# Performance work log

Measured on AMD Instinct MI355X. Metric: run time of the kernel, lower is better.

## Reference

```python
import jax, jax.numpy as jnp
import numpy as np

B, C, H, W = 16, 256, 96, 96
S, N = 128, 64  # num_s = 2*num_mid, num_n = num_mid
EPS = 1e-5


def _bn(x, g, b, m, v):
    # inference-mode BatchNorm2d over channel dim of x:[B,C,H,W]
    scale = g / jnp.sqrt(v + EPS)
    return (x - m[:, None, None]) * scale[:, None, None] + b[:, None, None]


def _proj(x, w, b, g, bb, m, v):
    # 1x1 conv + BN + ReLU (Basconv with is_batchnorm=True, kernel=1)
    y = jnp.einsum('bchw,oc->bohw', x, w) + b[:, None, None]
    return jax.nn.relu(_bn(y, g, bb, m, v))


def _gcn(x, w1, b1, w2):
    # x: [B, S, N]. conv1 acts on node dim (Conv1d over num_node channels),
    # residual add, LeakyReLU(0.2), conv2 acts on state dim (bias=False).
    h = jnp.einsum('bsn,mn->bsm', x, w1) + b1  # node mixing
    h = jax.nn.leaky_relu(h + x, 0.2)
    return jnp.einsum('bsn,ts->btn', h, w2)  # state mixing


def setup_inputs() -> dict:
    key = jax.random.key(0)
    ks = list(jax.random.split(key, 32))
    it = iter(ks)

    def nx(shape, s=0.05):
        return jax.random.normal(next(it), shape, jnp.float32) * s

    inp = {"x": jax.random.normal(next(it), (B, C, H, W), jnp.float32)}
    for name, o in [("s", S), ("p", N), ("r", N)]:
        inp[f"w_{name}"] = nx((o, C))
        inp[f"b_{name}"] = nx((o,))
        inp[f"bn_{name}_g"] = 1.0 + nx((o,))
        inp[f"bn_{name}_b"] = nx((o,))
        inp[f"bn_{name}_m"] = nx((o,))
        inp[f"bn_{name}_v"] = 0.5 + jax.random.uniform(next(it), (o,), jnp.float32)
    inp["g1_w1"] = nx((N, N)); inp["g1_b1"] = nx((N,)); inp["g1_w2"] = nx((S, S))
    inp["g2_w1"] = nx((N, N)); inp["g2_b1"] = nx((N,)); inp["g2_w2"] = nx((S, S))
    inp["fc2_w"] = nx((C, S))
    inp["bn_o_g"] = 1.0 + nx((C,))
    inp["bn_o_b"] = nx((C,))
    inp["bn_o_m"] = nx((C,))
    inp["bn_o_v"] = 0.5 + jax.random.uniform(next(it), (C,), jnp.float32)
    return inp


def reference(x, w_s, b_s, bn_s_g, bn_s_b, bn_s_m, bn_s_v,
              w_p, b_p, bn_p_g, bn_p_b, bn_p_m, bn_p_v,
              w_r, b_r, bn_r_g, bn_r_b, bn_r_m, bn_r_v,
              g1_w1, g1_b1, g1_w2, g2_w1, g2_b1, g2_w2,
              fc2_w, bn_o_g, bn_o_b, bn_o_m, bn_o_v):
    HW = H * W
    xs = _proj(x, w_s, b_s, bn_s_g, bn_s_b, bn_s_m, bn_s_v).reshape(B, S, HW)
    xp = _proj(x, w_p, b_p, bn_p_g, bn_p_b, bn_p_m, bn_p_v).reshape(B, N, HW)
    xr = _proj(x, w_r, b_r, bn_r_g, bn_r_b, bn_r_m, bn_r_v).reshape(B, N, HW)
    # project spatial features into latent graph: [B,S,N], normalized by HW
    g = jnp.einsum('bsl,bnl->bsn', xs, xp) * (1.0 / HW)
    g = _gcn(g, g1_w1, g1_b1, g1_w2)
    g = _gcn(g, g2_w1, g2_b1, g2_w2)
    # reproject latent graph back to spatial: [B,S,HW] -> [B,S,H,W]
    y = jnp.einsum('bsn,bnl->bsl', g, xr).reshape(B, S, H, W)
    y = jnp.einsum('bshw,cs->bchw', y, fc2_w)  # fc_2: 1x1 conv, no bias
    return x + _bn(y, bn_o_g, bn_o_b, bn_o_m, bn_o_v)
```

## Files before the change

### kernel.cpp

```cpp
#include <hip/hip_runtime.h>
#include <cstdint>
#include <cstddef>

#define B_ 16
#define C_ 256
#define HW_ 9216
#define S_ 128
#define N_ 64
#define LT_ 144
#define KSPLIT 12
#define LCHUNK 768

typedef __attribute__((ext_vector_type(8))) short bf16x8;
typedef __attribute__((ext_vector_type(4))) float f32x4;
typedef __attribute__((ext_vector_type(8))) unsigned short u16x8;

__device__ __forceinline__ unsigned short f2bf(float f) {
    unsigned int u = __builtin_bit_cast(unsigned int, f);
    u += 0x7fffu + ((u >> 16) & 1u);
    return (unsigned short)(u >> 16);
}
__device__ __forceinline__ float bf2f(unsigned short u) {
    unsigned int x = ((unsigned int)u) << 16;
    return __builtin_bit_cast(float, x);
}

__global__ void k0_prep(
    const float* __restrict__ w_s, const float* __restrict__ w_p, const float* __restrict__ w_r,
    const float* __restrict__ b_s, const float* __restrict__ g_s, const float* __restrict__ bb_s,
    const float* __restrict__ m_s, const float* __restrict__ v_s,
    const float* __restrict__ b_p, const float* __restrict__ g_p, const float* __restrict__ bb_p,
    const float* __restrict__ m_p, const float* __restrict__ v_p,
    const float* __restrict__ b_r, const float* __restrict__ g_r, const float* __restrict__ bb_r,
    const float* __restrict__ m_r, const float* __restrict__ v_r,
    const float* __restrict__ og, const float* __restrict__ ob,
    const float* __restrict__ om, const float* __restrict__ ov,
    unsigned short* __restrict__ Wcf, float* __restrict__ pscale, float* __restrict__ pbeta,
    float* __restrict__ oscale, float* __restrict__ obeta)
{
    const int gid = blockIdx.x * 256 + threadIdx.x;
    const int oc = gid >> 8, c = gid & 255;
    const float* wsrc;
    if (oc < 128)      wsrc = w_s + oc * 256;
    else if (oc < 192) wsrc = w_p + (oc - 128) * 256;
    else               wsrc = w_r + (oc - 192) * 256;
    Wcf[(c >> 3) * 2048 + oc * 8 + (c & 7)] = f2bf(wsrc[c]);
    if (gid < 256) {
        int i; const float *bp, *gp, *bbp, *mp, *vp;
        if (gid < 128)      { i = gid;       bp = b_s; gp = g_s; bbp = bb_s; mp = m_s; vp = v_s; }
        else if (gid < 192) { i = gid - 128; bp = b_p; gp = g_p; bbp = bb_p; mp = m_p; vp = v_p; }
        else                { i = gid - 192; bp = b_r; gp = g_r; bbp = bb_r; mp = m_r; vp = v_r; }
        const float sc = gp[i] / sqrtf(vp[i] + 1e-5f);
        pscale[gid] = sc;
        pbeta[gid]  = (bp[i] - mp[i]) * sc + bbp[i];
        const float so = og[gid] / sqrtf(ov[gid] + 1e-5f);
        oscale[gid] = so;
        obeta[gid]  = ob[gid] - om[gid] * so;
    }
}

__global__ void k0b_wbf(
    const float* __restrict__ g1w1, const float* __restrict__ g1w2,
    const float* __restrict__ g2w1, const float* __restrict__ g2w2,
    const float* __restrict__ fc2w, unsigned short* __restrict__ wbf)
{
    const int gid = blockIdx.x * 256 + threadIdx.x;
    float v;
    if (gid < 4096)       v = g1w1[gid];
    else if (gid < 20480) v = g1w2[gid - 4096];
    else if (gid < 24576) v = g2w1[gid - 20480];
    else if (gid < 40960) v = g2w2[gid - 24576];
    else                  v = fc2w[gid - 40960];
    wbf[gid] = f2bf(v);
}

__global__ __launch_bounds__(256, 3) void k1_proj(
    const float* __restrict__ x, const unsigned short* __restrict__ Wcf,
    const float* __restrict__ pscale, const float* __restrict__ pbeta,
    unsigned short* __restrict__ xsp, unsigned short* __restrict__ xrt)
{
    __shared__ unsigned short SH[18432];
    const int t = threadIdx.x;
    const int lane = t & 63;
    const int w = t >> 6;
    const int lt = blockIdx.x;
    const int b  = blockIdx.y;
    const int l0 = lt * 64;
    const float* xb = x + (size_t)b * C_ * HW_;
    const int lf = lane & 15;
    const int q4 = lane >> 4;
    const int kg0 = q4 * 8;
    const int r4 = q4 * 4;

    const int lq = t & 15;
    const int cs = t >> 4;
    const int c0 = cs * 4;

    f32x4 acc[4][4] = {};
    f32x4 Breg[4];

    #pragma unroll
    for (int j = 0; j < 4; ++j)
        Breg[j] = *(const f32x4*)(xb + (size_t)(c0 + j) * HW_ + l0 + lq * 4);

    for (int kt = 0; kt < 4; ++kt) {
        unsigned short* buf = SH + (kt & 1) * 4608;
        #pragma unroll
        for (int r = 0; r < 4; ++r) {
            const int ll = lq * 4 + r;
            ushort4 wv;
            wv.x = f2bf(Breg[0][r]); wv.y = f2bf(Breg[1][r]);
            wv.z = f2bf(Breg[2][r]); wv.w = f2bf(Breg[3][r]);
            *(ushort4*)&buf[ll * 72 + (c0 ^ ((lq & 7) << 3))] = wv;
        }
        __syncthreads();
        if (kt < 3) {
            const int k0n = (kt + 1) * 64;
            #pragma unroll
            for (int j = 0; j < 4; ++j)
                Breg[j] = *(const f32x4*)(xb + (size_t)(k0n + c0 + j) * HW_ + l0 + lq * 4);
        }
        #pragma unroll
        for (int ks = 0; ks < 2; ++ks) {
            const int kg = ks * 32 + kg0;
            bf16x8 al[4], bo[4];
            #pragma unroll
            for (int mi = 0; mi < 4; ++mi) {
                const int rr = mi * 16 + lf;
                al[mi] = *(const bf16x8*)&buf[rr * 72 + (kg ^ (((rr >> 2) & 7) << 3))];
            }
            const int chunk = kt * 8 + ks * 4 + q4;
            #pragma unroll
            for (int ni = 0; ni < 4; ++ni)
                bo[ni] = *(const bf16x8*)(Wcf + (size_t)chunk * 2048 + (w * 64 + ni * 16 + lf) * 8);
            #pragma unroll
            for (int mi = 0; mi < 4; ++mi)
                #pragma unroll
                for (int ni = 0; ni < 4; ++ni)
                    acc[mi][ni] = __builtin_amdgcn_mfma_f32_16x16x32_bf16(al[mi], bo[ni], acc[mi][ni], 0, 0, 0);
        }
        __syncthreads();
    }

    if (w < 3) {
        #pragma unroll
        for (int ni = 0; ni < 4; ++ni) {
            const int oc = w * 64 + ni * 16 + lf;
            const float sc = pscale[oc];
            const float bt = pbeta[oc];
            #pragma unroll
            for (int mi = 0; mi < 4; ++mi) {
                const int lcol = mi * 16 + r4;
                ushort4 pk;
                #pragma unroll
                for (int r = 0; r < 4; ++r) {
                    float y = acc[mi][ni][r] * sc + bt;
                    y = y > 0.f ? y : 0.f;
                    ((unsigned short*)&pk)[r] = f2bf(y);
                }
                *(ushort4*)&SH[oc * 72 + lcol] = pk;
            }
        }
    } else {
        #pragma unroll
        for (int ni = 0; ni < 4; ++ni) {
            const int oc = 192 + ni * 16 + lf;
            const float sc = pscale[oc];
            const float bt = pbeta[oc];
            const int n = ni * 16 + lf;
            #pragma unroll
            for (int mi = 0; mi < 4; ++mi) {
                const int lbase = mi * 16 + r4;
                #pragma unroll
                for (int r = 0; r < 4; ++r) {
                    float y = acc[mi][ni][r] * sc + bt;
                    y = y > 0.f ? y : 0.f;
                    xrt[((size_t)b * HW_ + l0 + lbase + r) * 64 + n] = f2bf(y);
                }
            }
        }
    }
    __syncthreads();

    #pragma unroll
    for (int i = 0; i < 6; ++i) {
        const int id = t + i * 256;
        const int row = id >> 3;
        const int c8 = (id & 7) * 8;
        const u16x8 v = *(const u16x8*)&SH[row * 72 + c8];
        *(u16x8*)(xsp + ((size_t)b * 192 + row) * HW_ + l0 + c8) = v;
    }
}

__global__ __launch_bounds__(256) void k2_gram(
    const unsigned short* __restrict__ xsp, float* __restrict__ gpart)
{
    __shared__ unsigned short As[128 * 136];
    __shared__ unsigned short Bs[64 * 136];
    const int t = threadIdx.x;
    const int lane = t & 63;
    const int w = t >> 6;
    const int ck = blockIdx.x;
    const int b = blockIdx.y;

    f32x4 acc[2][4] = {};

    for (int it = 0; it < 6; ++it) {
        const int lg = ck * LCHUNK + it * 128;
        {
            const int rr = t >> 4;
            const int lq2 = (t & 15) * 8;
            #pragma unroll
            for (int i = 0; i < 8; ++i) {
                const int s = rr + 16 * i;
                *(u16x8*)&As[s * 136 + lq2] =
                    *(const u16x8*)(xsp + ((size_t)b * 192 + s) * HW_ + lg + lq2);
            }
            #pragma unroll
            for (int i = 0; i < 4; ++i) {
                const int n = rr + 16 * i;
                *(u16x8*)&Bs[n * 136 + lq2] =
                    *(const u16x8*)(xsp + ((size_t)b * 192 + 128 + n) * HW_ + lg + lq2);
            }
        }
        __syncthreads();
        #pragma unroll
        for (int ks = 0; ks < 4; ++ks) {
            const int kg = ks * 32 + (lane >> 4) * 8;
            bf16x8 a[2], bv[4];
            #pragma unroll
            for (int mi = 0; mi < 2; ++mi)
                a[mi] = *(const bf16x8*)&As[(w * 32 + mi * 16 + (lane & 15)) * 136 + kg];
            #pragma unroll
            for (int ni = 0; ni < 4; ++ni)
                bv[ni] = *(const bf16x8*)&Bs[(ni * 16 + (lane & 15)) * 136 + kg];
            #pragma unroll
            for (int mi = 0; mi < 2; ++mi)
                #pragma unroll
                for (int ni = 0; ni < 4; ++ni)
                    acc[mi][ni] = __builtin_amdgcn_mfma_f32_16x16x32_bf16(a[mi], bv[ni], acc[mi][ni], 0, 0, 0);
        }
        __syncthreads();
    }
    float* gp = gpart + (size_t)(ck * 16 + b) * (S_ * N_);
    const int lf = lane & 15, r4 = (lane >> 4) * 4;
    #pragma unroll
    for (int mi = 0; mi < 2; ++mi)
        #pragma unroll
        for (int ni = 0; ni < 4; ++ni)
            #pragma unroll
            for (int r = 0; r < 4; ++r) {
                const int s = w * 32 + mi * 16 + r4 + r;
                const int n = ni * 16 + lf;
                gp[s * 64 + n] = acc[mi][ni][r];
            }
}

__global__ __launch_bounds__(128) void kred(
    const float* __restrict__ gpart, unsigned short* __restrict__ gred)
{
    const int id = blockIdx.x * 128 + threadIdx.x;
    f32x4 s = {};
    const float* p = gpart + (size_t)id * 4;
    #pragma unroll
    for (int ck = 0; ck < KSPLIT; ++ck)
        s += *(const f32x4*)(p + (size_t)ck * 16 * (S_ * N_));
    s *= (1.0f / (float)HW_);
    ushort4 h;
    h.x = f2bf(s[0]); h.y = f2bf(s[1]); h.z = f2bf(s[2]); h.w = f2bf(s[3]);
    *(ushort4*)&gred[(size_t)id * 4] = h;
}

__global__ __launch_bounds__(256) void k_gcn(
    const unsigned short* __restrict__ gred, const unsigned short* __restrict__ wbf,
    const float* __restrict__ b1a, const float* __restrict__ b1b,
    unsigned short* __restrict__ hc)
{
    __shared__ unsigned short G[128 * 72];
    __shared__ unsigned short HT[64 * 136];
    __shared__ unsigned short T2[64 * 136];
    const int b = blockIdx.x;
    const int t = threadIdx.x;
    const int lane = t & 63;
    const int w = t >> 6;
    const int lf = lane & 15;
    const int kg0 = (lane >> 4) * 8;
    const int r4 = (lane >> 4) * 4;

    const unsigned short* w1a = wbf;
    const unsigned short* w2a = wbf + 4096;
    const unsigned short* w1b = wbf + 20480;
    const unsigned short* w2b = wbf + 24576;
    const unsigned short* fc2 = wbf + 40960;

    #pragma unroll
    for (int i = 0; i < 4; ++i) {
        const int chunk = t + i * 256;
        const u16x8 v = *(const u16x8*)(gred + (size_t)b * (S_ * N_) + chunk * 8);
        const int s = chunk >> 3, n = (chunk & 7) * 8;
        *(u16x8*)&G[s * 72 + n] = v;
    }
    __syncthreads();

    for (int pass = 0; pass < 2; ++pass) {
        const unsigned short* w1 = pass ? w1b : w1a;
        const unsigned short* w2 = pass ? w2b : w2a;
        const float* b1 = pass ? b1b : b1a;

        {
            f32x4 acc[2][4] = {};
            #pragma unroll
            for (int ks = 0; ks < 2; ++ks) {
                const int kg = ks * 32 + kg0;
                bf16x8 a[2], bv[4];
                #pragma unroll
                for (int mi = 0; mi < 2; ++mi)
                    a[mi] = *(const bf16x8*)&G[(w * 32 + mi * 16 + lf) * 72 + kg];
                #pragma unroll
                for (int ni = 0; ni < 4; ++ni)
                    bv[ni] = *(const bf16x8*)(w1 + (ni * 16 + lf) * 64 + kg);
                #pragma unroll
                for (int mi = 0; mi < 2; ++mi)
                    #pragma unroll
                    for (int ni = 0; ni < 4; ++ni)
                        acc[mi][ni] = __builtin_amdgcn_mfma_f32_16x16x32_bf16(a[mi], bv[ni], acc[mi][ni], 0, 0, 0);
            }
            #pragma unroll
            for (int mi = 0; mi < 2; ++mi) {
                const int s0 = w * 32 + mi * 16 + r4;
                #pragma unroll
                for (int ni = 0; ni < 4; ++ni) {
                    const int m = ni * 16 + lf;
                    const float bm = b1[m];
                    ushort4 pk;
                    #pragma unroll
                    for (int r = 0; r < 4; ++r) {
                        float v = acc[mi][ni][r] + bm + bf2f(G[(s0 + r) * 72 + m]);
                        v = v > 0.f ? v : 0.2f * v;
                        ((unsigned short*)&pk)[r] = f2bf(v);
                    }
                    *(ushort4*)&HT[m * 136 + s0] = pk;
                }
            }
        }
        __syncthreads();

        {
            f32x4 acc[2][4] = {};
            #pragma unroll
            for (int ks = 0; ks < 4; ++ks) {
                const int kg = ks * 32 + kg0;
                bf16x8 a[2], bv[4];
                #pragma unroll
                for (int mi = 0; mi < 2; ++mi)
                    a[mi] = *(const bf16x8*)(w2 + (w * 32 + mi * 16 + lf) * 128 + kg);
                #pragma unroll
                for (int ni = 0; ni < 4; ++ni)
                    bv[ni] = *(const bf16x8*)&HT[(ni * 16 + lf) * 136 + kg];
                #pragma unroll
                for (int mi = 0; mi < 2; ++mi)
                    #pragma unroll
                    for (int ni = 0; ni < 4; ++ni)
                        acc[mi][ni] = __builtin_amdgcn_mfma_f32_16x16x32_bf16(a[mi], bv[ni], acc[mi][ni], 0, 0, 0);
            }
            if (pass == 0) {
                #pragma unroll
                for (int mi = 0; mi < 2; ++mi) {
                    const int t0 = w * 32 + mi * 16 + r4;
                    #pragma unroll
                    for (int ni = 0; ni < 4; ++ni) {
                        const int m = ni * 16 + lf;
                        #pragma unroll
                        for (int r = 0; r < 4; ++r)
                            G[(t0 + r) * 72 + m] = f2bf(acc[mi][ni][r]);
                    }
                }
            } else {
                #pragma unroll
                for (int mi = 0; mi < 2; ++mi) {
                    const int t0 = w * 32 + mi * 16 + r4;
                    #pragma unroll
                    for (int ni = 0; ni < 4; ++ni) {
                        const int m = ni * 16 + lf;
                        ushort4 pk;
                        #pragma unroll
                        for (int r = 0; r < 4; ++r)
                            ((unsigned short*)&pk)[r] = f2bf(acc[mi][ni][r]);
                        *(ushort4*)&T2[m * 136 + t0] = pk;
                    }
                }
            }
        }
        __syncthreads();
    }

    {
        f32x4 acc[4][4] = {};
        #pragma unroll
        for (int ks = 0; ks < 4; ++ks) {
            const int kg = ks * 32 + kg0;
            bf16x8 a[4], bv[4];
            #pragma unroll
            for (int mi = 0; mi < 4; ++mi)
                a[mi] = *(const bf16x8*)(fc2 + (w * 64 + mi * 16 + lf) * 128 + kg);
            #pragma unroll
            for (int ni = 0; ni < 4; ++ni)
                bv[ni] = *(const bf16x8*)&T2[(ni * 16 + lf) * 136 + kg];
            #pragma unroll
            for (int mi = 0; mi < 4; ++mi)
                #pragma unroll
                for (int ni = 0; ni < 4; ++ni)
                    acc[mi][ni] = __builtin_amdgcn_mfma_f32_16x16x32_bf16(a[mi], bv[ni], acc[mi][ni], 0, 0, 0);
        }
        #pragma unroll
        for (int mi = 0; mi < 4; ++mi) {
            const int c0 = w * 64 + mi * 16 + r4;
            #pragma unroll
            for (int ni = 0; ni < 4; ++ni) {
                const int n = ni * 16 + lf;
                #pragma unroll
                for (int r = 0; r < 4; ++r)
                    hc[((size_t)b * 256 + c0 + r) * 64 + n] = f2bf(acc[mi][ni][r]);
            }
        }
    }
}

__global__ __launch_bounds__(256) void k3_out(
    const float* __restrict__ x, const unsigned short* __restrict__ hc,
    const unsigned short* __restrict__ xrt,
    const float* __restrict__ oscale, const float* __restrict__ obeta,
    float* __restrict__ out)
{
    const int t = threadIdx.x;
    const int lane = t & 63;
    const int w = t >> 6;
    const int wr = w >> 1, wc = w & 1;
    const int l0 = blockIdx.x * 128;
    const int moff = blockIdx.y * 128;
    const int b = blockIdx.z;
    const int lf = lane & 15;
    const int q4 = lane >> 4;
    const int kg0 = q4 * 8;
    const int r4 = q4 * 4;

    const unsigned short* hb = hc + (size_t)b * 256 * 64 + (size_t)(moff + wr * 64) * 64;
    const unsigned short* xrb = xrt + ((size_t)b * HW_ + l0 + wc * 64) * 64;

    f32x4 acc[4][4] = {};
    #pragma unroll
    for (int ks = 0; ks < 2; ++ks) {
        const int kg = ks * 32 + kg0;
        bf16x8 al[4], bc[4];
        #pragma unroll
        for (int mi = 0; mi < 4; ++mi)
            al[mi] = *(const bf16x8*)(xrb + (size_t)(mi * 16 + lf) * 64 + kg);
        #pragma unroll
        for (int ni = 0; ni < 4; ++ni)
            bc[ni] = *(const bf16x8*)(hb + (size_t)(ni * 16 + lf) * 64 + kg);
        #pragma unroll
        for (int mi = 0; mi < 4; ++mi)
            #pragma unroll
            for (int ni = 0; ni < 4; ++ni)
                acc[mi][ni] = __builtin_amdgcn_mfma_f32_16x16x32_bf16(al[mi], bc[ni], acc[mi][ni], 0, 0, 0);
    }
    #pragma unroll
    for (int ni = 0; ni < 4; ++ni) {
        const int c = moff + wr * 64 + ni * 16 + lf;
        const float sc = oscale[c];
        const float bt = obeta[c];
        const size_t rowb = ((size_t)b * 256 + c) * HW_;
        #pragma unroll
        for (int mi = 0; mi < 4; ++mi) {
            const int l = l0 + wc * 64 + mi * 16 + r4;
            const f32x4 xv = *(const f32x4*)(x + rowb + l);
            f32x4 o;
            #pragma unroll
            for (int r = 0; r < 4; ++r)
                o[r] = xv[r] + acc[mi][ni][r] * sc + bt;
            *(f32x4*)(out + rowb + l) = o;
        }
    }
}

extern "C" void kernel_launch(void* const* d_in, const int* in_sizes, int n_in,
                              void* d_out, int out_size, void* d_ws, size_t ws_size,
                              hipStream_t stream) {
    (void)in_sizes; (void)n_in; (void)out_size;
    const float* x     = (const float*)d_in[0];
    const float* w_s   = (const float*)d_in[1];
    const float* b_s   = (const float*)d_in[2];
    const float* g_s   = (const float*)d_in[3];
    const float* bb_s  = (const float*)d_in[4];
    const float* m_s   = (const float*)d_in[5];
    const float* v_s   = (const float*)d_in[6];
    const float* w_p   = (const float*)d_in[7];
    const float* b_p   = (const float*)d_in[8];
    const float* g_p   = (const float*)d_in[9];
    const float* bb_p  = (const float*)d_in[10];
    const float* m_p   = (const float*)d_in[11];
    const float* v_p   = (const float*)d_in[12];
    const float* w_r   = (const float*)d_in[13];
    const float* b_r   = (const float*)d_in[14];
    const float* g_r   = (const float*)d_in[15];
    const float* bb_r  = (const float*)d_in[16];
    const float* m_r   = (const float*)d_in[17];
    const float* v_r   = (const float*)d_in[18];
    const float* g1w1  = (const float*)d_in[19];
    const float* g1b1  = (const float*)d_in[20];
    const float* g1w2  = (const float*)d_in[21];
    const float* g2w1  = (const float*)d_in[22];
    const float* g2b1  = (const float*)d_in[23];
    const float* g2w2  = (const float*)d_in[24];
    const float* fc2w  = (const float*)d_in[25];
    const float* bn_og = (const float*)d_in[26];
    const float* bn_ob = (const float*)d_in[27];
    const float* bn_om = (const float*)d_in[28];
    const float* bn_ov = (const float*)d_in[29];

    char* ws = (char*)d_ws;
    unsigned short* Wcf = (unsigned short*)(ws + 0);
    float* pscale = (float*)(ws + 131072);
    float* pbeta  = (float*)(ws + 132096);
    float* oscale = (float*)(ws + 133120);
    float* obeta  = (float*)(ws + 134144);
    unsigned short* wbf = (unsigned short*)(ws + 135168);
    const size_t o_fix = 135168 + 147456;
    const size_t sz_xsp = (size_t)B_ * 192 * HW_ * 2;
    const size_t sz_xrt = (size_t)B_ * HW_ * 64 * 2;
    const size_t sz_gp  = (size_t)KSPLIT * B_ * S_ * N_ * 4;
    const size_t sz_gr  = (size_t)B_ * S_ * N_ * 2;
    const size_t sz_hc  = (size_t)B_ * 256 * 64 * 2;
    const size_t need_full = o_fix + sz_xsp + sz_xrt + sz_gp + sz_gr + sz_hc;

    unsigned short* xsp; size_t o2;
    if (ws_size >= need_full) { xsp = (unsigned short*)(ws + o_fix); o2 = o_fix + sz_xsp; }
    else {
        xsp = (unsigned short*)d_out; o2 = o_fix;
    }
    unsigned short* xrt  = (unsigned short*)(ws + o2);
    float* gpart         = (float*)(ws + o2 + sz_xrt);
    unsigned short* gred = (unsigned short*)(ws + o2 + sz_xrt + sz_gp);
    unsigned short* hc   = (unsigned short*)(ws + o2 + sz_xrt + sz_gp + sz_gr);

    k0_prep<<<256, 256, 0, stream>>>(
        w_s, w_p, w_r,
        b_s, g_s, bb_s, m_s, v_s,
        b_p, g_p, bb_p, m_p, v_p,
        b_r, g_r, bb_r, m_r, v_r,
        bn_og, bn_ob, bn_om, bn_ov,
        Wcf, pscale, pbeta, oscale, obeta);

    k0b_wbf<<<288, 256, 0, stream>>>(g1w1, g1w2, g2w1, g2w2, fc2w, wbf);

    k1_proj<<<dim3(LT_, B_), 256, 0, stream>>>(x, Wcf, pscale, pbeta, xsp, xrt);

    k2_gram<<<dim3(KSPLIT, B_), 256, 0, stream>>>(xsp, gpart);

    kred<<<256, 128, 0, stream>>>(gpart, gred);

    k_gcn<<<16, 256, 0, stream>>>(gred, wbf, g1b1, g2b1, hc);

    k3_out<<<dim3(72, 2, 16), 256, 0, stream>>>(x, hc, xrt, oscale, obeta, (float*)d_out);
}
```

Measured before the change: 160.0 us.

## Hoist all x loads in projection, fuse split-K reduction into GCN, prefetch residual

The projection kernel now issues all four K-tiles of x loads up front, stages them into shared memory once, and runs the whole MFMA loop after a single barrier. The old design alternated per-tile loads, conversions and barriers. The separate split-K reduction kernel is removed, and k_gcn sums the fp32 partials directly, which saves a launch and the bf16 intermediate buffer. The output kernel prefetches half of the residual x tiles before the MFMA work to hide load latency. The cost is higher register pressure (64 floats of staged x plus the prefetch) and more serial reduction work inside the 16-block GCN kernel.

```diff
diff --git a/kernel.cpp b/kernel.cpp
--- a/kernel.cpp
+++ b/kernel.cpp
@@ -95,52 +95,49 @@
     const int lq = t & 15;
     const int cs = t >> 4;
     const int c0 = cs * 4;
-
-    f32x4 acc[4][4] = {};
-    f32x4 Breg[4];
-
-    #pragma unroll
-    for (int j = 0; j < 4; ++j)
-        Breg[j] = *(const f32x4*)(xb + (size_t)(c0 + j) * HW_ + l0 + lq * 4);
-
-    for (int kt = 0; kt < 4; ++kt) {
-        unsigned short* buf = SH + (kt & 1) * 4608;
+    const int cswz = c0 ^ ((lq & 7) << 3);
+
+    f32x4 Breg[4][4];
+    #pragma unroll
+    for (int kt = 0; kt < 4; ++kt)
+        #pragma unroll
+        for (int j = 0; j < 4; ++j)
+            Breg[kt][j] = *(const f32x4*)(xb + (size_t)(kt * 64 + c0 + j) * HW_ + l0 + lq * 4);
+
+    #pragma unroll
+    for (int kt = 0; kt < 4; ++kt)
         #pragma unroll
         for (int r = 0; r < 4; ++r) {
             const int ll = lq * 4 + r;
             ushort4 wv;
-            wv.x = f2bf(Breg[0][r]); wv.y = f2bf(Breg[1][r]);
-            wv.z = f2bf(Breg[2][r]); wv.w = f2bf(Breg[3][r]);
-            *(ushort4*)&buf[ll * 72 + (c0 ^ ((lq & 7) << 3))] = wv;
-        }
-        __syncthreads();
-        if (kt < 3) {
-            const int k0n = (kt + 1) * 64;
-            #pragma unroll
-            for (int j = 0; j < 4; ++j)
-                Breg[j] = *(const f32x4*)(xb + (size_t)(k0n + c0 + j) * HW_ + l0 + lq * 4);
-        }
-        #pragma unroll
-        for (int ks = 0; ks < 2; ++ks) {
-            const int kg = ks * 32 + kg0;
-            bf16x8 al[4], bo[4];
-            #pragma unroll
-            for (int mi = 0; mi < 4; ++mi) {
-                const int rr = mi * 16 + lf;
-                al[mi] = *(const bf16x8*)&buf[rr * 72 + (kg ^ (((rr >> 2) & 7) << 3))];
-            }
-            const int chunk = kt * 8 + ks * 4 + q4;
+            wv.x = f2bf(Breg[kt][0][r]); wv.y = f2bf(Breg[kt][1][r]);
+            wv.z = f2bf(Breg[kt][2][r]); wv.w = f2bf(Breg[kt][3][r]);
+            *(ushort4*)&SH[kt * 4608 + ll * 72 + cswz] = wv;
+        }
+    __syncthreads();
+
+    f32x4 acc[4][4] = {};
+    #pragma unroll
+    for (int ks = 0; ks < 8; ++ks) {
+        const int kt = ks >> 1;
+        const int kg = (ks & 1) * 32 + kg0;
+        bf16x8 al[4], bo[4];
+        #pragma unroll
+        for (int mi = 0; mi < 4; ++mi) {
+            const int rr = mi * 16 + lf;
+            al[mi] = *(const bf16x8*)&SH[kt * 4608 + rr * 72 + (kg ^ (((rr >> 2) & 7) << 3))];
+        }
+        const int chunk = ks * 4 + q4;
+        #pragma unroll
+        for (int ni = 0; ni < 4; ++ni)
+            bo[ni] = *(const bf16x8*)(Wcf + (size_t)chunk * 2048 + (w * 64 + ni * 16 + lf) * 8);
+        #pragma unroll
+        for (int mi = 0; mi < 4; ++mi)
             #pragma unroll
             for (int ni = 0; ni < 4; ++ni)
-                bo[ni] = *(const bf16x8*)(Wcf + (size_t)chunk * 2048 + (w * 64 + ni * 16 + lf) * 8);
-            #pragma unroll
-            for (int mi = 0; mi < 4; ++mi)
-                #pragma unroll
-                for (int ni = 0; ni < 4; ++ni)
-                    acc[mi][ni] = __builtin_amdgcn_mfma_f32_16x16x32_bf16(al[mi], bo[ni], acc[mi][ni], 0, 0, 0);
-        }
-        __syncthreads();
-    }
+                acc[mi][ni] = __builtin_amdgcn_mfma_f32_16x16x32_bf16(al[mi], bo[ni], acc[mi][ni], 0, 0, 0);
+    }
+    __syncthreads();
 
     if (w < 3) {
         #pragma unroll
@@ -256,23 +253,8 @@
             }
 }
 
-__global__ __launch_bounds__(128) void kred(
-    const float* __restrict__ gpart, unsigned short* __restrict__ gred)
-{
-    const int id = blockIdx.x * 128 + threadIdx.x;
-    f32x4 s = {};
-    const float* p = gpart + (size_t)id * 4;
-    #pragma unroll
-    for (int ck = 0; ck < KSPLIT; ++ck)
-        s += *(const f32x4*)(p + (size_t)ck * 16 * (S_ * N_));
-    s *= (1.0f / (float)HW_);
-    ushort4 h;
-    h.x = f2bf(s[0]); h.y = f2bf(s[1]); h.z = f2bf(s[2]); h.w = f2bf(s[3]);
-    *(ushort4*)&gred[(size_t)id * 4] = h;
-}
-
 __global__ __launch_bounds__(256) void k_gcn(
-    const unsigned short* __restrict__ gred, const unsigned short* __restrict__ wbf,
+    const float* __restrict__ gpart, const unsigned short* __restrict__ wbf,
     const float* __restrict__ b1a, const float* __restrict__ b1b,
     unsigned short* __restrict__ hc)
 {
@@ -294,11 +276,18 @@
     const unsigned short* fc2 = wbf + 40960;
 
     #pragma unroll
-    for (int i = 0; i < 4; ++i) {
-        const int chunk = t + i * 256;
-        const u16x8 v = *(const u16x8*)(gred + (size_t)b * (S_ * N_) + chunk * 8);
-        const int s = chunk >> 3, n = (chunk & 7) * 8;
-        *(u16x8*)&G[s * 72 + n] = v;
+    for (int j = 0; j < 8; ++j) {
+        const int v = t + j * 256;
+        f32x4 s = {};
+        #pragma unroll
+        for (int ck = 0; ck < KSPLIT; ++ck)
+            s += *(const f32x4*)(gpart + (size_t)(ck * 16 + b) * (S_ * N_) + v * 4);
+        s *= (1.0f / (float)HW_);
+        const int e = v * 4;
+        const int sr = e >> 6, nc = e & 63;
+        ushort4 h;
+        h.x = f2bf(s[0]); h.y = f2bf(s[1]); h.z = f2bf(s[2]); h.w = f2bf(s[3]);
+        *(ushort4*)&G[sr * 72 + nc] = h;
     }
     __syncthreads();
 
@@ -447,6 +436,15 @@
     const unsigned short* hb = hc + (size_t)b * 256 * 64 + (size_t)(moff + wr * 64) * 64;
     const unsigned short* xrb = xrt + ((size_t)b * HW_ + l0 + wc * 64) * 64;
 
+    f32x4 xpre[8];
+    #pragma unroll
+    for (int p = 0; p < 8; ++p) {
+        const int ni = p >> 2, mi = p & 3;
+        const int c = moff + wr * 64 + ni * 16 + lf;
+        const int l = l0 + wc * 64 + mi * 16 + r4;
+        xpre[p] = *(const f32x4*)(x + ((size_t)b * 256 + c) * HW_ + l);
+    }
+
     f32x4 acc[4][4] = {};
     #pragma unroll
     for (int ks = 0; ks < 2; ++ks) {
@@ -473,7 +471,8 @@
         #pragma unroll
         for (int mi = 0; mi < 4; ++mi) {
             const int l = l0 + wc * 64 + mi * 16 + r4;
-            const f32x4 xv = *(const f32x4*)(x + rowb + l);
+            const f32x4 xv = (ni < 2) ? xpre[ni * 4 + mi]
+                                      : *(const f32x4*)(x + rowb + l);
             f32x4 o;
             #pragma unroll
             for (int r = 0; r < 4; ++r)
@@ -529,19 +528,17 @@
     const size_t sz_xsp = (size_t)B_ * 192 * HW_ * 2;
     const size_t sz_xrt = (size_t)B_ * HW_ * 64 * 2;
     const size_t sz_gp  = (size_t)KSPLIT * B_ * S_ * N_ * 4;
-    const size_t sz_gr  = (size_t)B_ * S_ * N_ * 2;
     const size_t sz_hc  = (size_t)B_ * 256 * 64 * 2;
-    const size_t need_full = o_fix + sz_xsp + sz_xrt + sz_gp + sz_gr + sz_hc;
+    const size_t need_full = o_fix + sz_xsp + sz_xrt + sz_gp + sz_hc;
 
     unsigned short* xsp; size_t o2;
     if (ws_size >= need_full) { xsp = (unsigned short*)(ws + o_fix); o2 = o_fix + sz_xsp; }
     else {
         xsp = (unsigned short*)d_out; o2 = o_fix;
     }
-    unsigned short* xrt  = (unsigned short*)(ws + o2);
-    float* gpart         = (float*)(ws + o2 + sz_xrt);
-    unsigned short* gred = (unsigned short*)(ws + o2 + sz_xrt + sz_gp);
-    unsigned short* hc   = (unsigned short*)(ws + o2 + sz_xrt + sz_gp + sz_gr);
+    unsigned short* xrt = (unsigned short*)(ws + o2);
+    float* gpart        = (float*)(ws + o2 + sz_xrt);
+    unsigned short* hc  = (unsigned short*)(ws + o2 + sz_xrt + sz_gp);
 
     k0_prep<<<256, 256, 0, stream>>>(
         w_s, w_p, w_r,
@@ -557,9 +554,7 @@
 
     k2_gram<<<dim3(KSPLIT, B_), 256, 0, stream>>>(xsp, gpart);
 
-    kred<<<256, 128, 0, stream>>>(gpart, gred);
-
-    k_gcn<<<16, 256, 0, stream>>>(gred, wbf, g1b1, g2b1, hc);
+    k_gcn<<<16, 256, 0, stream>>>(gpart, wbf, g1b1, g2b1, hc);
 
     k3_out<<<dim3(72, 2, 16), 256, 0, stream>>>(x, hc, xrt, oscale, obeta, (float*)d_out);
 }
```

After: 163.7 us. +2.3%, slower.

## Fuse Gram partial products into projection kernel and drop xs/xp intermediate

Applied to the files above, without the earlier changes.

The projection kernel now computes per-tile partial Gram matrices (xs·xpᵀ over its 64 spatial positions) directly from shared memory and writes them as bf16 partials. The separate gram kernel and the large xs/xp round trip through global memory go away. The reduction kernel now sums 144 bf16 partials per batch instead of 12 fp32 ones, which adds partial-write traffic and more rounding error. The output kernel also prefetches part of x before its MFMA loop to hide load latency.

```diff
diff --git a/kernel.cpp b/kernel.cpp
--- a/kernel.cpp
+++ b/kernel.cpp
@@ -8,8 +8,6 @@
 #define S_ 128
 #define N_ 64
 #define LT_ 144
-#define KSPLIT 12
-#define LCHUNK 768
 
 typedef __attribute__((ext_vector_type(8))) short bf16x8;
 typedef __attribute__((ext_vector_type(4))) float f32x4;
@@ -77,7 +75,7 @@
 __global__ __launch_bounds__(256, 3) void k1_proj(
     const float* __restrict__ x, const unsigned short* __restrict__ Wcf,
     const float* __restrict__ pscale, const float* __restrict__ pbeta,
-    unsigned short* __restrict__ xsp, unsigned short* __restrict__ xrt)
+    unsigned short* __restrict__ xrt, unsigned short* __restrict__ gpb)
 {
     __shared__ unsigned short SH[18432];
     const int t = threadIdx.x;
@@ -182,92 +180,55 @@
     }
     __syncthreads();
 
-    #pragma unroll
-    for (int i = 0; i < 6; ++i) {
-        const int id = t + i * 256;
-        const int row = id >> 3;
-        const int c8 = (id & 7) * 8;
-        const u16x8 v = *(const u16x8*)&SH[row * 72 + c8];
-        *(u16x8*)(xsp + ((size_t)b * 192 + row) * HW_ + l0 + c8) = v;
-    }
-}
-
-__global__ __launch_bounds__(256) void k2_gram(
-    const unsigned short* __restrict__ xsp, float* __restrict__ gpart)
+    {
+        f32x4 acc2[4][2] = {};
+        #pragma unroll
+        for (int ks = 0; ks < 2; ++ks) {
+            const int kg = ks * 32 + kg0;
+            bf16x8 an[4], bs_[2];
+            #pragma unroll
+            for (int mi = 0; mi < 4; ++mi)
+                an[mi] = *(const bf16x8*)&SH[(128 + mi * 16 + lf) * 72 + kg];
+            #pragma unroll
+            for (int ni = 0; ni < 2; ++ni)
+                bs_[ni] = *(const bf16x8*)&SH[(w * 32 + ni * 16 + lf) * 72 + kg];
+            #pragma unroll
+            for (int mi = 0; mi < 4; ++mi)
+                #pragma unroll
+                for (int ni = 0; ni < 2; ++ni)
+                    acc2[mi][ni] = __builtin_amdgcn_mfma_f32_16x16x32_bf16(an[mi], bs_[ni], acc2[mi][ni], 0, 0, 0);
+        }
+        unsigned short* gp = gpb + (size_t)(lt * 16 + b) * (S_ * N_);
+        #pragma unroll
+        for (int ni = 0; ni < 2; ++ni) {
+            const int s = w * 32 + ni * 16 + lf;
+            #pragma unroll
+            for (int mi = 0; mi < 4; ++mi) {
+                ushort4 pk;
+                #pragma unroll
+                for (int r = 0; r < 4; ++r)
+                    ((unsigned short*)&pk)[r] = f2bf(acc2[mi][ni][r]);
+                *(ushort4*)&gp[s * 64 + mi * 16 + r4] = pk;
+            }
+        }
+    }
+}
+
+__global__ __launch_bounds__(256) void kred(
+    const unsigned short* __restrict__ gpb, unsigned short* __restrict__ gred)
 {
-    __shared__ unsigned short As[128 * 136];
-    __shared__ unsigned short Bs[64 * 136];
-    const int t = threadIdx.x;
-    const int lane = t & 63;
-    const int w = t >> 6;
-    const int ck = blockIdx.x;
-    const int b = blockIdx.y;
-
-    f32x4 acc[2][4] = {};
-
-    for (int it = 0; it < 6; ++it) {
-        const int lg = ck * LCHUNK + it * 128;
-        {
-            const int rr = t >> 4;
-            const int lq2 = (t & 15) * 8;
-            #pragma unroll
-            for (int i = 0; i < 8; ++i) {
-                const int s = rr + 16 * i;
-                *(u16x8*)&As[s * 136 + lq2] =
-                    *(const u16x8*)(xsp + ((size_t)b * 192 + s) * HW_ + lg + lq2);
-            }
-            #pragma unroll
-            for (int i = 0; i < 4; ++i) {
-                const int n = rr + 16 * i;
-                *(u16x8*)&Bs[n * 136 + lq2] =
-                    *(const u16x8*)(xsp + ((size_t)b * 192 + 128 + n) * HW_ + lg + lq2);
-            }
-        }
-        __syncthreads();
-        #pragma unroll
-        for (int ks = 0; ks < 4; ++ks) {
-            const int kg = ks * 32 + (lane >> 4) * 8;
-            bf16x8 a[2], bv[4];
-            #pragma unroll
-            for (int mi = 0; mi < 2; ++mi)
-                a[mi] = *(const bf16x8*)&As[(w * 32 + mi * 16 + (lane & 15)) * 136 + kg];
-            #pragma unroll
-            for (int ni = 0; ni < 4; ++ni)
-                bv[ni] = *(const bf16x8*)&Bs[(ni * 16 + (lane & 15)) * 136 + kg];
-            #pragma unroll
-            for (int mi = 0; mi < 2; ++mi)
-                #pragma unroll
-                for (int ni = 0; ni < 4; ++ni)
-                    acc[mi][ni] = __builtin_amdgcn_mfma_f32_16x16x32_bf16(a[mi], bv[ni], acc[mi][ni], 0, 0, 0);
-        }
-        __syncthreads();
-    }
-    float* gp = gpart + (size_t)(ck * 16 + b) * (S_ * N_);
-    const int lf = lane & 15, r4 = (lane >> 4) * 4;
-    #pragma unroll
-    for (int mi = 0; mi < 2; ++mi)
-        #pragma unroll
-        for (int ni = 0; ni < 4; ++ni)
-            #pragma unroll
-            for (int r = 0; r < 4; ++r) {
-                const int s = w * 32 + mi * 16 + r4 + r;
-                const int n = ni * 16 + lf;
-                gp[s * 64 + n] = acc[mi][ni][r];
-            }
-}
-
-__global__ __launch_bounds__(128) void kred(
-    const float* __restrict__ gpart, unsigned short* __restrict__ gred)
-{
-    const int id = blockIdx.x * 128 + threadIdx.x;
-    f32x4 s = {};
-    const float* p = gpart + (size_t)id * 4;
-    #pragma unroll
-    for (int ck = 0; ck < KSPLIT; ++ck)
-        s += *(const f32x4*)(p + (size_t)ck * 16 * (S_ * N_));
-    s *= (1.0f / (float)HW_);
+    const int id = blockIdx.x * 256 + threadIdx.x;
+    float s0 = 0.f, s1 = 0.f, s2 = 0.f, s3 = 0.f;
+    const unsigned short* p = gpb + (size_t)id * 4;
+    #pragma unroll 8
+    for (int lt = 0; lt < LT_; ++lt) {
+        const ushort4 v = *(const ushort4*)(p + (size_t)lt * 16 * (S_ * N_));
+        s0 += bf2f(v.x); s1 += bf2f(v.y); s2 += bf2f(v.z); s3 += bf2f(v.w);
+    }
+    const float inv = 1.0f / (float)HW_;
     ushort4 h;
-    h.x = f2bf(s[0]); h.y = f2bf(s[1]); h.z = f2bf(s[2]); h.w = f2bf(s[3]);
+    h.x = f2bf(s0 * inv); h.y = f2bf(s1 * inv);
+    h.z = f2bf(s2 * inv); h.w = f2bf(s3 * inv);
     *(ushort4*)&gred[(size_t)id * 4] = h;
 }
 
@@ -447,6 +408,15 @@
     const unsigned short* hb = hc + (size_t)b * 256 * 64 + (size_t)(moff + wr * 64) * 64;
     const unsigned short* xrb = xrt + ((size_t)b * HW_ + l0 + wc * 64) * 64;
 
+    f32x4 xpre[8];
+    #pragma unroll
+    for (int p = 0; p < 8; ++p) {
+        const int ni = p >> 2, mi = p & 3;
+        const int c = moff + wr * 64 + ni * 16 + lf;
+        const int l = l0 + wc * 64 + mi * 16 + r4;
+        xpre[p] = *(const f32x4*)(x + ((size_t)b * 256 + c) * HW_ + l);
+    }
+
     f32x4 acc[4][4] = {};
     #pragma unroll
     for (int ks = 0; ks < 2; ++ks) {
@@ -473,7 +443,8 @@
         #pragma unroll
         for (int mi = 0; mi < 4; ++mi) {
             const int l = l0 + wc * 64 + mi * 16 + r4;
-            const f32x4 xv = *(const f32x4*)(x + rowb + l);
+            const f32x4 xv = (ni < 2) ? xpre[ni * 4 + mi]
+                                      : *(const f32x4*)(x + rowb + l);
             f32x4 o;
             #pragma unroll
             for (int r = 0; r < 4; ++r)
@@ -526,22 +497,20 @@
     float* obeta  = (float*)(ws + 134144);
     unsigned short* wbf = (unsigned short*)(ws + 135168);
     const size_t o_fix = 135168 + 147456;
-    const size_t sz_xsp = (size_t)B_ * 192 * HW_ * 2;
     const size_t sz_xrt = (size_t)B_ * HW_ * 64 * 2;
-    const size_t sz_gp  = (size_t)KSPLIT * B_ * S_ * N_ * 4;
     const size_t sz_gr  = (size_t)B_ * S_ * N_ * 2;
     const size_t sz_hc  = (size_t)B_ * 256 * 64 * 2;
-    const size_t need_full = o_fix + sz_xsp + sz_xrt + sz_gp + sz_gr + sz_hc;
-
-    unsigned short* xsp; size_t o2;
-    if (ws_size >= need_full) { xsp = (unsigned short*)(ws + o_fix); o2 = o_fix + sz_xsp; }
-    else {
-        xsp = (unsigned short*)d_out; o2 = o_fix;
-    }
-    unsigned short* xrt  = (unsigned short*)(ws + o2);
-    float* gpart         = (float*)(ws + o2 + sz_xrt);
-    unsigned short* gred = (unsigned short*)(ws + o2 + sz_xrt + sz_gp);
-    unsigned short* hc   = (unsigned short*)(ws + o2 + sz_xrt + sz_gp + sz_gr);
+    const size_t sz_gpb = (size_t)LT_ * B_ * S_ * N_ * 2;
+    const size_t need_full = o_fix + sz_xrt + sz_gr + sz_hc + sz_gpb;
+
+    unsigned short* xrt  = (unsigned short*)(ws + o_fix);
+    unsigned short* gred = (unsigned short*)(ws + o_fix + sz_xrt);
+    unsigned short* hc   = (unsigned short*)(ws + o_fix + sz_xrt + sz_gr);
+    unsigned short* gpb;
+    if (ws_size >= need_full)
+        gpb = (unsigned short*)(ws + o_fix + sz_xrt + sz_gr + sz_hc);
+    else
+        gpb = (unsigned short*)d_out;
 
     k0_prep<<<256, 256, 0, stream>>>(
         w_s, w_p, w_r,
@@ -553,11 +522,9 @@
 
     k0b_wbf<<<288, 256, 0, stream>>>(g1w1, g1w2, g2w1, g2w2, fc2w, wbf);
 
-    k1_proj<<<dim3(LT_, B_), 256, 0, stream>>>(x, Wcf, pscale, pbeta, xsp, xrt);
-
-    k2_gram<<<dim3(KSPLIT, B_), 256, 0, stream>>>(xsp, gpart);
-
-    kred<<<256, 128, 0, stream>>>(gpart, gred);
+    k1_proj<<<dim3(LT_, B_), 256, 0, stream>>>(x, Wcf, pscale, pbeta, xrt, gpb);
+
+    kred<<<128, 256, 0, stream>>>(gpb, gred);
 
     k_gcn<<<16, 256, 0, stream>>>(gred, wbf, g1b1, g2b1, hc);
 
```

After: 156.0 us. 2.5% less time.
